# Kernel tuning notes

Measured on AMD Instinct MI355X. Metric: run time of the kernel, lower is better.

Reference implementation:

```python
import jax, jax.numpy as jnp
import numpy as np

NUM_LAYERS = 16
IN_SIZE = 1024
OUT_SIZE = 1024
B, S = 64, 128

def setup_inputs() -> dict:
    key = jax.random.key(0)
    k1, k2, k3 = jax.random.split(key, 3)
    x = jax.random.normal(k1, (B, S, IN_SIZE), dtype=jnp.float32)
    layer_idx = jax.random.randint(k2, (S,), 0, NUM_LAYERS)
    weight = jax.random.normal(k3, (NUM_LAYERS, OUT_SIZE, IN_SIZE), dtype=jnp.float32)
    return {"x": x, "layer_idx": layer_idx, "weight": weight}

def reference(x, layer_idx, weight):
    # Branch: layer_idx is 1D with len == S (per-position weight selection).
    # Gather per-position weights [S, O, D] and do one batched contraction,
    # equivalent to the Python loop of per-step matmuls in the original.
    w = weight[layer_idx]                       # [S, O, D]
    out = jnp.einsum('bsd,sod->bso', x, w)      # [B, S, O]
    return out
```

## Files before the change

### kernel.cpp

```cpp
#include <hip/hip_runtime.h>
#include <hip/hip_bf16.h>

#define B_ 64
#define S_ 128
#define D_ 1024
#define O_ 1024
#define L_ 16

typedef __bf16 bf16x8 __attribute__((ext_vector_type(8)));
typedef float f32x4 __attribute__((ext_vector_type(4)));

#define WS_W   0ull
#define WS_X   33554432ull
#define WS_P   50331648ull
#define WS_NEED (50331664ull + 72ull * 16ull)

__device__ __forceinline__ unsigned f2bf2(float a, float b) {
    union { float f; unsigned u; } x{a}, y{b};
    unsigned lo = x.u + 0x7FFFu + ((x.u >> 16) & 1u);
    unsigned hi = y.u + 0x7FFFu + ((y.u >> 16) & 1u);
    return (lo >> 16) | (hi & 0xFFFF0000u);
}

__device__ __forceinline__ void gload16(const void* g, void* l) {
    __builtin_amdgcn_global_load_lds(
        (const __attribute__((address_space(1))) void*)g,
        (__attribute__((address_space(3))) void*)l, 16, 0, 0);
}

__global__ __launch_bounds__(256) void moshi_convert(
    const float* __restrict__ x, const float* __restrict__ w,
    const int* __restrict__ lidx, unsigned char* __restrict__ ws) {
    if (blockIdx.x == 0 && threadIdx.x < 16) {
        int t = threadIdx.x;
        int cnt[16];
        #pragma unroll 1
        for (int m = 0; m < 16; ++m) cnt[m] = 0;
        for (int s = 0; s < S_; ++s) ++cnt[lidx[s]];
        int off = 0;
        for (int m = 0; m < t; ++m) off += (cnt[m] + 1) >> 1;
        int4* pairs = (int4*)(ws + WS_P + 16);
        int k = 0, prev = -1;
        for (int s = 0; s < S_; ++s) {
            if (lidx[s] == t) {
                if (k & 1) pairs[off + (k >> 1)] = make_int4(prev, s, t, 0);
                prev = s; ++k;
            }
        }
        if (k & 1) pairs[off + (k >> 1)] = make_int4(prev, prev, t, 0);
        if (t == 0) {
            int tot = 0;
            for (int m = 0; m < 16; ++m) tot += (cnt[m] + 1) >> 1;
            *(int*)(ws + WS_P) = tot;
        }
    }
    const float4* src;
    uint2* dst;
    unsigned i0 = blockIdx.x * 512 + threadIdx.x;
    if (blockIdx.x < 8192) {
        src = reinterpret_cast<const float4*>(w);
        dst = reinterpret_cast<uint2*>(ws + WS_W);
    } else {
        src = reinterpret_cast<const float4*>(x);
        dst = reinterpret_cast<uint2*>(ws + WS_X);
        i0 -= 4194304u;
    }
    float4 v0 = src[i0];
    float4 v1 = src[i0 + 256];
    dst[i0]       = make_uint2(f2bf2(v0.x, v0.y), f2bf2(v0.z, v0.w));
    dst[i0 + 256] = make_uint2(f2bf2(v1.x, v1.y), f2bf2(v1.z, v1.w));
}

__global__ __launch_bounds__(512, 4) void moshi_gemm_n128(
    const unsigned char* __restrict__ ws, float* __restrict__ out) {
    __shared__ __align__(16) unsigned char lw[16384];
    __shared__ __align__(16) unsigned char lx[16384];

    const int bid = (blockIdx.x & 7) * 72 + (blockIdx.x >> 3);
    const int pi = bid >> 3;
    const int nt = bid & 7;
    const int np = *reinterpret_cast<const int*>(ws + WS_P);
    if (pi >= np) return;
    const int4 pr = *reinterpret_cast<const int4*>(ws + WS_P + 16 + 16ull * pi);
    const int s0 = pr.x, s1 = pr.y, l = pr.z;

    const int tid = threadIdx.x, lane = tid & 63, wid = tid >> 6;

    const int rowq = tid >> 3;
    const int c16  = (tid & 7) << 4;
    const int csw  = c16 ^ ((rowq & 7) << 4);
    const unsigned char* wsrc0 = ws + WS_W
        + ((size_t)(l * 1024 + nt * 128 + rowq) << 11) + csw;
    const unsigned char* wsrc1 = wsrc0 + ((size_t)64 << 11);
    const unsigned char* xsrc0 = ws + WS_X
        + ((size_t)(rowq * 128 + s0) << 11) + csw;
    const unsigned char* xsrc1 = ws + WS_X
        + ((size_t)(rowq * 128 + s1) << 11) + csw;

    const int wm = wid >> 2, wn = wid & 3;
    const int swz = (lane & 7) << 4;
    const int kb  = (lane >> 4) << 4;
    const int a_base = (wm * 64 + (lane & 15)) * 128 + kb;
    const int b_base = (wn * 32 + (lane & 15)) * 128 + kb;

    f32x4 acc[4][2];
    #pragma unroll
    for (int i = 0; i < 4; ++i)
        #pragma unroll
        for (int j = 0; j < 2; ++j) acc[i][j] = (f32x4)0.0f;

    #pragma unroll 1
    for (int kt = 0; kt < 16; ++kt) {
        __syncthreads();
        gload16(wsrc0 + kt * 128, lw + tid * 16);
        gload16(wsrc1 + kt * 128, lw + tid * 16 + 8192);
        gload16(xsrc0 + kt * 128, lx + tid * 16);
        gload16(xsrc1 + kt * 128, lx + tid * 16 + 8192);
        __syncthreads();
        #pragma unroll
        for (int kk = 0; kk < 2; ++kk) {
            bf16x8 af[4], bfr[2];
            #pragma unroll
            for (int mi = 0; mi < 4; ++mi)
                af[mi] = *reinterpret_cast<const bf16x8*>(
                    lx + (((a_base + kk * 64) ^ swz) + mi * 2048));
            #pragma unroll
            for (int ni = 0; ni < 2; ++ni)
                bfr[ni] = *reinterpret_cast<const bf16x8*>(
                    lw + (((b_base + kk * 64) ^ swz) + ni * 2048));
            #pragma unroll
            for (int mi = 0; mi < 4; ++mi)
                #pragma unroll
                for (int ni = 0; ni < 2; ++ni)
                    acc[mi][ni] = __builtin_amdgcn_mfma_f32_16x16x32_bf16(
                        af[mi], bfr[ni], acc[mi][ni], 0, 0, 0);
        }
    }

    const int s_sel = wm ? s1 : s0;
    const int col0 = nt * 128 + wn * 32 + (lane & 15);
    const int r0 = (lane >> 4) << 2;
    #pragma unroll
    for (int mi = 0; mi < 4; ++mi)
        #pragma unroll
        for (int ni = 0; ni < 2; ++ni)
            #pragma unroll
            for (int r = 0; r < 4; ++r) {
                int b = mi * 16 + r0 + r;
                out[((size_t)b * S_ + s_sel) * O_ + col0 + ni * 16] = acc[mi][ni][r];
            }
}

__global__ __launch_bounds__(256) void moshi_flin_fallback(
    const float* __restrict__ x, const int* __restrict__ lidx,
    const float* __restrict__ w, float* __restrict__ out) {
    __shared__ __align__(16) unsigned char lxs[64 * 128];
    __shared__ __align__(16) unsigned char lws[128 * 128];
    const int bid = blockIdx.x;
    const int s = bid >> 3, n0 = (bid & 7) << 7;
    const int tid = threadIdx.x, lane = tid & 63, wid = tid >> 6;
    const int idx = lidx[s];
    const float* wb = w + (size_t)idx * O_ * D_ + (size_t)n0 * D_;
    const float* xb = x + (size_t)s * D_;
    const int swz = (lane & 7) << 4;
    const int kb = (lane >> 4) << 4;
    const int a_base = (lane & 15) * 128 + kb;
    const int b_base = (wid * 32 + (lane & 15)) * 128 + kb;
    f32x4 acc[4][2];
    #pragma unroll
    for (int i = 0; i < 4; ++i)
        #pragma unroll
        for (int j = 0; j < 2; ++j) acc[i][j] = (f32x4)0.0f;
    for (int kt = 0; kt < D_; kt += 64) {
        __syncthreads();
        #pragma unroll
        for (int p = 0; p < 4; ++p) {
            int f = tid + p * 256, row = f >> 4, cc = (f & 15) << 2;
            const float4 v = *reinterpret_cast<const float4*>(
                xb + (size_t)row * (S_ * D_) + kt + cc);
            uint2 pk = { f2bf2(v.x, v.y), f2bf2(v.z, v.w) };
            *reinterpret_cast<uint2*>(&lxs[(row * 128 + cc * 2) ^ ((row & 7) << 4)]) = pk;
        }
        #pragma unroll
        for (int p = 0; p < 8; ++p) {
            int f = tid + p * 256, row = f >> 4, cc = (f & 15) << 2;
            const float4 v = *reinterpret_cast<const float4*>(
                wb + (size_t)row * D_ + kt + cc);
            uint2 pk = { f2bf2(v.x, v.y), f2bf2(v.z, v.w) };
            *reinterpret_cast<uint2*>(&lws[(row * 128 + cc * 2) ^ ((row & 7) << 4)]) = pk;
        }
        __syncthreads();
        #pragma unroll
        for (int kk = 0; kk < 2; ++kk) {
            bf16x8 af[4], bfr[2];
            #pragma unroll
            for (int mi = 0; mi < 4; ++mi)
                af[mi] = *reinterpret_cast<const bf16x8*>(
                    &lxs[(((a_base + kk * 64) ^ swz) + mi * 2048)]);
            #pragma unroll
            for (int ni = 0; ni < 2; ++ni)
                bfr[ni] = *reinterpret_cast<const bf16x8*>(
                    &lws[(((b_base + kk * 64) ^ swz) + ni * 2048)]);
            #pragma unroll
            for (int mi = 0; mi < 4; ++mi)
                #pragma unroll
                for (int ni = 0; ni < 2; ++ni)
                    acc[mi][ni] = __builtin_amdgcn_mfma_f32_16x16x32_bf16(
                        af[mi], bfr[ni], acc[mi][ni], 0, 0, 0);
        }
    }
    float* ob = out + (size_t)s * O_ + n0 + wid * 32 + (lane & 15);
    const int r0 = (lane >> 4) << 2;
    #pragma unroll
    for (int mi = 0; mi < 4; ++mi)
        #pragma unroll
        for (int ni = 0; ni < 2; ++ni)
            #pragma unroll
            for (int r = 0; r < 4; ++r) {
                int b = mi * 16 + r0 + r;
                ob[(size_t)b * (S_ * O_) + ni * 16] = acc[mi][ni][r];
            }
}

extern "C" void kernel_launch(void* const* d_in, const int* in_sizes, int n_in,
                              void* d_out, int out_size, void* d_ws, size_t ws_size,
                              hipStream_t stream) {
    const float* x  = (const float*)d_in[0];
    const int* lidx = (const int*)d_in[1];
    const float* w  = (const float*)d_in[2];
    float* out      = (float*)d_out;

    if (ws_size < WS_NEED) {
        moshi_flin_fallback<<<dim3(128 * 8), dim3(256), 0, stream>>>(x, lidx, w, out);
        return;
    }
    unsigned char* ws = (unsigned char*)d_ws;
    moshi_convert<<<dim3(12288), dim3(256), 0, stream>>>(x, w, lidx, ws);
    moshi_gemm_n128<<<dim3(72 * 8), dim3(512), 0, stream>>>(ws, out);
}
```

Before: 56.29 us.

## Use atomic work queue per N-tile and transpose x to s-major bf16 layout

The GEMM now launches 512 persistent blocks that take pair work items from per-N-tile atomic counters, replacing the fixed 576-block grid where blocks beyond the pair count exit early. The convert kernel now writes x in [s][b][d] order, so the 64 batch rows for one position are contiguous, and it zeroes the queue counters. The aim is better load balance and more local x reads, at the cost of atomics and extra block-wide barriers per item.

```diff
diff --git a/kernel.cpp b/kernel.cpp
--- a/kernel.cpp
+++ b/kernel.cpp
@@ -10,10 +10,12 @@
 typedef __bf16 bf16x8 __attribute__((ext_vector_type(8)));
 typedef float f32x4 __attribute__((ext_vector_type(4)));
 
-#define WS_W   0ull
-#define WS_X   33554432ull
-#define WS_P   50331648ull
-#define WS_NEED (50331664ull + 72ull * 16ull)
+#define WS_W     0ull
+#define WS_X     33554432ull
+#define WS_P     50331648ull
+#define WS_PAIRS (WS_P + 16ull)
+#define WS_Q     (WS_PAIRS + 72ull * 16ull)
+#define WS_NEED  (WS_Q + 32ull)
 
 __device__ __forceinline__ unsigned f2bf2(float a, float b) {
     union { float f; unsigned u; } x{a}, y{b};
@@ -31,124 +33,142 @@
 __global__ __launch_bounds__(256) void moshi_convert(
     const float* __restrict__ x, const float* __restrict__ w,
     const int* __restrict__ lidx, unsigned char* __restrict__ ws) {
-    if (blockIdx.x == 0 && threadIdx.x < 16) {
-        int t = threadIdx.x;
-        int cnt[16];
-        #pragma unroll 1
-        for (int m = 0; m < 16; ++m) cnt[m] = 0;
-        for (int s = 0; s < S_; ++s) ++cnt[lidx[s]];
-        int off = 0;
-        for (int m = 0; m < t; ++m) off += (cnt[m] + 1) >> 1;
-        int4* pairs = (int4*)(ws + WS_P + 16);
-        int k = 0, prev = -1;
-        for (int s = 0; s < S_; ++s) {
-            if (lidx[s] == t) {
-                if (k & 1) pairs[off + (k >> 1)] = make_int4(prev, s, t, 0);
-                prev = s; ++k;
-            }
-        }
-        if (k & 1) pairs[off + (k >> 1)] = make_int4(prev, prev, t, 0);
-        if (t == 0) {
-            int tot = 0;
-            for (int m = 0; m < 16; ++m) tot += (cnt[m] + 1) >> 1;
-            *(int*)(ws + WS_P) = tot;
-        }
-    }
-    const float4* src;
-    uint2* dst;
+    if (blockIdx.x == 0 && threadIdx.x < 24) {
+        if (threadIdx.x >= 16) {
+            ((int*)(ws + WS_Q))[threadIdx.x - 16] = 0;
+        } else {
+            int t = threadIdx.x;
+            int cnt[16];
+            #pragma unroll 1
+            for (int m = 0; m < 16; ++m) cnt[m] = 0;
+            for (int s = 0; s < S_; ++s) ++cnt[lidx[s]];
+            int off = 0;
+            for (int m = 0; m < t; ++m) off += (cnt[m] + 1) >> 1;
+            int4* pairs = (int4*)(ws + WS_PAIRS);
+            int k = 0, prev = -1;
+            for (int s = 0; s < S_; ++s) {
+                if (lidx[s] == t) {
+                    if (k & 1) pairs[off + (k >> 1)] = make_int4(prev, s, t, 0);
+                    prev = s; ++k;
+                }
+            }
+            if (k & 1) pairs[off + (k >> 1)] = make_int4(prev, prev, t, 0);
+            if (t == 0) {
+                int tot = 0;
+                for (int m = 0; m < 16; ++m) tot += (cnt[m] + 1) >> 1;
+                *(int*)(ws + WS_P) = tot;
+            }
+        }
+    }
     unsigned i0 = blockIdx.x * 512 + threadIdx.x;
     if (blockIdx.x < 8192) {
-        src = reinterpret_cast<const float4*>(w);
-        dst = reinterpret_cast<uint2*>(ws + WS_W);
+        const float4* src = reinterpret_cast<const float4*>(w);
+        uint2* dst = reinterpret_cast<uint2*>(ws + WS_W);
+        float4 v0 = src[i0];
+        float4 v1 = src[i0 + 256];
+        dst[i0]       = make_uint2(f2bf2(v0.x, v0.y), f2bf2(v0.z, v0.w));
+        dst[i0 + 256] = make_uint2(f2bf2(v1.x, v1.y), f2bf2(v1.z, v1.w));
     } else {
-        src = reinterpret_cast<const float4*>(x);
-        dst = reinterpret_cast<uint2*>(ws + WS_X);
-        i0 -= 4194304u;
-    }
-    float4 v0 = src[i0];
-    float4 v1 = src[i0 + 256];
-    dst[i0]       = make_uint2(f2bf2(v0.x, v0.y), f2bf2(v0.z, v0.w));
-    dst[i0 + 256] = make_uint2(f2bf2(v1.x, v1.y), f2bf2(v1.z, v1.w));
-}
-
-__global__ __launch_bounds__(512, 4) void moshi_gemm_n128(
+        const float4* src = reinterpret_cast<const float4*>(x);
+        uint2* dst = reinterpret_cast<uint2*>(ws + WS_X);
+        unsigned j = i0 - 4194304u;
+        float4 v0 = src[j];
+        float4 v1 = src[j + 256];
+        unsigned b0 = j >> 15, s0 = (j >> 8) & 127u, d40 = j & 255u;
+        dst[(s0 * 64u + b0) * 256u + d40] =
+            make_uint2(f2bf2(v0.x, v0.y), f2bf2(v0.z, v0.w));
+        unsigned j1 = j + 256u;
+        unsigned b1 = j1 >> 15, s1 = (j1 >> 8) & 127u, d41 = j1 & 255u;
+        dst[(s1 * 64u + b1) * 256u + d41] =
+            make_uint2(f2bf2(v1.x, v1.y), f2bf2(v1.z, v1.w));
+    }
+}
+
+__global__ __launch_bounds__(512, 4) void moshi_gemm_pq(
     const unsigned char* __restrict__ ws, float* __restrict__ out) {
     __shared__ __align__(16) unsigned char lw[16384];
     __shared__ __align__(16) unsigned char lx[16384];
-
-    const int bid = (blockIdx.x & 7) * 72 + (blockIdx.x >> 3);
-    const int pi = bid >> 3;
-    const int nt = bid & 7;
+    __shared__ int item_s;
+
+    const int nt = blockIdx.x & 7;
+    int* ctr = (int*)(ws + WS_Q) + nt;
     const int np = *reinterpret_cast<const int*>(ws + WS_P);
-    if (pi >= np) return;
-    const int4 pr = *reinterpret_cast<const int4*>(ws + WS_P + 16 + 16ull * pi);
-    const int s0 = pr.x, s1 = pr.y, l = pr.z;
 
     const int tid = threadIdx.x, lane = tid & 63, wid = tid >> 6;
-
     const int rowq = tid >> 3;
     const int c16  = (tid & 7) << 4;
     const int csw  = c16 ^ ((rowq & 7) << 4);
-    const unsigned char* wsrc0 = ws + WS_W
-        + ((size_t)(l * 1024 + nt * 128 + rowq) << 11) + csw;
-    const unsigned char* wsrc1 = wsrc0 + ((size_t)64 << 11);
-    const unsigned char* xsrc0 = ws + WS_X
-        + ((size_t)(rowq * 128 + s0) << 11) + csw;
-    const unsigned char* xsrc1 = ws + WS_X
-        + ((size_t)(rowq * 128 + s1) << 11) + csw;
-
     const int wm = wid >> 2, wn = wid & 3;
     const int swz = (lane & 7) << 4;
     const int kb  = (lane >> 4) << 4;
     const int a_base = (wm * 64 + (lane & 15)) * 128 + kb;
     const int b_base = (wn * 32 + (lane & 15)) * 128 + kb;
 
-    f32x4 acc[4][2];
-    #pragma unroll
-    for (int i = 0; i < 4; ++i)
-        #pragma unroll
-        for (int j = 0; j < 2; ++j) acc[i][j] = (f32x4)0.0f;
-
-    #pragma unroll 1
-    for (int kt = 0; kt < 16; ++kt) {
-        __syncthreads();
-        gload16(wsrc0 + kt * 128, lw + tid * 16);
-        gload16(wsrc1 + kt * 128, lw + tid * 16 + 8192);
-        gload16(xsrc0 + kt * 128, lx + tid * 16);
-        gload16(xsrc1 + kt * 128, lx + tid * 16 + 8192);
-        __syncthreads();
-        #pragma unroll
-        for (int kk = 0; kk < 2; ++kk) {
-            bf16x8 af[4], bfr[2];
-            #pragma unroll
-            for (int mi = 0; mi < 4; ++mi)
-                af[mi] = *reinterpret_cast<const bf16x8*>(
-                    lx + (((a_base + kk * 64) ^ swz) + mi * 2048));
+    const unsigned char* wbase = ws + WS_W + ((size_t)(nt * 128 + rowq) << 11) + csw;
+
+    for (;;) {
+        if (tid == 0) item_s = atomicAdd(ctr, 1);
+        __syncthreads();
+        const int pi = item_s;
+        __syncthreads();
+        if (pi >= 72) break;
+        if (pi >= np) continue;
+
+        const int4 pr = *reinterpret_cast<const int4*>(ws + WS_PAIRS + 16ull * pi);
+        const int s0 = pr.x, s1 = pr.y, l = pr.z;
+
+        const unsigned char* wsrc0 = wbase + ((size_t)(l * 1024) << 11);
+        const unsigned char* wsrc1 = wsrc0 + ((size_t)64 << 11);
+        const unsigned char* xsrc0 = ws + WS_X + ((size_t)(s0 * 64 + rowq) << 11) + csw;
+        const unsigned char* xsrc1 = ws + WS_X + ((size_t)(s1 * 64 + rowq) << 11) + csw;
+
+        f32x4 acc[4][2];
+        #pragma unroll
+        for (int i = 0; i < 4; ++i)
+            #pragma unroll
+            for (int j = 0; j < 2; ++j) acc[i][j] = (f32x4)0.0f;
+
+        #pragma unroll 1
+        for (int kt = 0; kt < 16; ++kt) {
+            __syncthreads();
+            gload16(wsrc0 + kt * 128, lw + tid * 16);
+            gload16(wsrc1 + kt * 128, lw + tid * 16 + 8192);
+            gload16(xsrc0 + kt * 128, lx + tid * 16);
+            gload16(xsrc1 + kt * 128, lx + tid * 16 + 8192);
+            __syncthreads();
+            #pragma unroll
+            for (int kk = 0; kk < 2; ++kk) {
+                bf16x8 af[4], bfr[2];
+                #pragma unroll
+                for (int mi = 0; mi < 4; ++mi)
+                    af[mi] = *reinterpret_cast<const bf16x8*>(
+                        lx + (((a_base + kk * 64) ^ swz) + mi * 2048));
+                #pragma unroll
+                for (int ni = 0; ni < 2; ++ni)
+                    bfr[ni] = *reinterpret_cast<const bf16x8*>(
+                        lw + (((b_base + kk * 64) ^ swz) + ni * 2048));
+                #pragma unroll
+                for (int mi = 0; mi < 4; ++mi)
+                    #pragma unroll
+                    for (int ni = 0; ni < 2; ++ni)
+                        acc[mi][ni] = __builtin_amdgcn_mfma_f32_16x16x32_bf16(
+                            af[mi], bfr[ni], acc[mi][ni], 0, 0, 0);
+            }
+        }
+
+        const int s_sel = wm ? s1 : s0;
+        const int col0 = nt * 128 + wn * 32 + (lane & 15);
+        const int r0 = (lane >> 4) << 2;
+        #pragma unroll
+        for (int mi = 0; mi < 4; ++mi)
             #pragma unroll
             for (int ni = 0; ni < 2; ++ni)
-                bfr[ni] = *reinterpret_cast<const bf16x8*>(
-                    lw + (((b_base + kk * 64) ^ swz) + ni * 2048));
-            #pragma unroll
-            for (int mi = 0; mi < 4; ++mi)
-                #pragma unroll
-                for (int ni = 0; ni < 2; ++ni)
-                    acc[mi][ni] = __builtin_amdgcn_mfma_f32_16x16x32_bf16(
-                        af[mi], bfr[ni], acc[mi][ni], 0, 0, 0);
-        }
-    }
-
-    const int s_sel = wm ? s1 : s0;
-    const int col0 = nt * 128 + wn * 32 + (lane & 15);
-    const int r0 = (lane >> 4) << 2;
-    #pragma unroll
-    for (int mi = 0; mi < 4; ++mi)
-        #pragma unroll
-        for (int ni = 0; ni < 2; ++ni)
-            #pragma unroll
-            for (int r = 0; r < 4; ++r) {
-                int b = mi * 16 + r0 + r;
-                out[((size_t)b * S_ + s_sel) * O_ + col0 + ni * 16] = acc[mi][ni][r];
-            }
+                #pragma unroll
+                for (int r = 0; r < 4; ++r) {
+                    int b = mi * 16 + r0 + r;
+                    out[((size_t)b * S_ + s_sel) * O_ + col0 + ni * 16] = acc[mi][ni][r];
+                }
+    }
 }
 
 __global__ __launch_bounds__(256) void moshi_flin_fallback(
@@ -236,5 +256,5 @@
     }
     unsigned char* ws = (unsigned char*)d_ws;
     moshi_convert<<<dim3(12288), dim3(256), 0, stream>>>(x, w, lidx, ws);
-    moshi_gemm_n128<<<dim3(72 * 8), dim3(512), 0, stream>>>(ws, out);
-}
+    moshi_gemm_pq<<<dim3(512), dim3(512), 0, stream>>>(ws, out);
+}
```

Result: slower. 75.11 us (+33.4%).

## Pre-pack x into MFMA fragment layout and load A operands directly from global

Applied to the files above, without the earlier changes.

The convert kernel now writes bf16 x in a per-position layout that matches the MFMA A-fragment order, so each lane can read its fragments with one 16-byte global load. The GEMM kernel drops the x shared-memory tile and its staging loads, keeping only the weight tile in LDS. The aim is to cut LDS traffic and shared memory use, which may raise occupancy. In exchange, A operands come straight from global or cache with latency exposed inside the k loop, and the convert kernel's stores become scattered.

```diff
diff --git a/kernel.cpp b/kernel.cpp
--- a/kernel.cpp
+++ b/kernel.cpp
@@ -9,11 +9,13 @@
 
 typedef __bf16 bf16x8 __attribute__((ext_vector_type(8)));
 typedef float f32x4 __attribute__((ext_vector_type(4)));
-
-#define WS_W   0ull
-#define WS_X   33554432ull
-#define WS_P   50331648ull
-#define WS_NEED (50331664ull + 72ull * 16ull)
+typedef unsigned u32x4 __attribute__((ext_vector_type(4)));
+
+#define WS_W     0ull
+#define WS_X     33554432ull
+#define WS_P     50331648ull
+#define WS_PAIRS (WS_P + 16ull)
+#define WS_NEED  (WS_PAIRS + 72ull * 16ull)
 
 __device__ __forceinline__ unsigned f2bf2(float a, float b) {
     union { float f; unsigned u; } x{a}, y{b};
@@ -39,7 +41,7 @@
         for (int s = 0; s < S_; ++s) ++cnt[lidx[s]];
         int off = 0;
         for (int m = 0; m < t; ++m) off += (cnt[m] + 1) >> 1;
-        int4* pairs = (int4*)(ws + WS_P + 16);
+        int4* pairs = (int4*)(ws + WS_PAIRS);
         int k = 0, prev = -1;
         for (int s = 0; s < S_; ++s) {
             if (lidx[s] == t) {
@@ -54,54 +56,56 @@
             *(int*)(ws + WS_P) = tot;
         }
     }
-    const float4* src;
-    uint2* dst;
-    unsigned i0 = blockIdx.x * 512 + threadIdx.x;
     if (blockIdx.x < 8192) {
-        src = reinterpret_cast<const float4*>(w);
-        dst = reinterpret_cast<uint2*>(ws + WS_W);
+        unsigned i0 = blockIdx.x * 512u + threadIdx.x;
+        const float4* src = reinterpret_cast<const float4*>(w);
+        uint2* dst = reinterpret_cast<uint2*>(ws + WS_W);
+        float4 v0 = src[i0];
+        float4 v1 = src[i0 + 256];
+        dst[i0]       = make_uint2(f2bf2(v0.x, v0.y), f2bf2(v0.z, v0.w));
+        dst[i0 + 256] = make_uint2(f2bf2(v1.x, v1.y), f2bf2(v1.z, v1.w));
     } else {
-        src = reinterpret_cast<const float4*>(x);
-        dst = reinterpret_cast<uint2*>(ws + WS_X);
-        i0 -= 4194304u;
-    }
-    float4 v0 = src[i0];
-    float4 v1 = src[i0 + 256];
-    dst[i0]       = make_uint2(f2bf2(v0.x, v0.y), f2bf2(v0.z, v0.w));
-    dst[i0 + 256] = make_uint2(f2bf2(v1.x, v1.y), f2bf2(v1.z, v1.w));
-}
-
-__global__ __launch_bounds__(512, 4) void moshi_gemm_n128(
+        unsigned p = (blockIdx.x - 8192u) * 256u + threadIdx.x;
+        const float4* src = reinterpret_cast<const float4*>(x);
+        float4 v0 = src[2u * p];
+        float4 v1 = src[2u * p + 1u];
+        unsigned b = p >> 14, s = (p >> 7) & 127u, d8 = p & 127u;
+        unsigned kt = d8 >> 3, kk = (d8 >> 2) & 1u, lh = d8 & 3u;
+        unsigned mi = b >> 4, ml = b & 15u;
+        unsigned dstb = s * 131072u + (((kt * 2u + kk) * 4u + mi) << 10)
+                      + ((ml + lh * 16u) << 4);
+        u32x4 pk = { f2bf2(v0.x, v0.y), f2bf2(v0.z, v0.w),
+                     f2bf2(v1.x, v1.y), f2bf2(v1.z, v1.w) };
+        *reinterpret_cast<u32x4*>(ws + WS_X + dstb) = pk;
+    }
+}
+
+__global__ __launch_bounds__(512, 4) void moshi_gemm_xd(
     const unsigned char* __restrict__ ws, float* __restrict__ out) {
     __shared__ __align__(16) unsigned char lw[16384];
-    __shared__ __align__(16) unsigned char lx[16384];
 
     const int bid = (blockIdx.x & 7) * 72 + (blockIdx.x >> 3);
     const int pi = bid >> 3;
     const int nt = bid & 7;
     const int np = *reinterpret_cast<const int*>(ws + WS_P);
     if (pi >= np) return;
-    const int4 pr = *reinterpret_cast<const int4*>(ws + WS_P + 16 + 16ull * pi);
+    const int4 pr = *reinterpret_cast<const int4*>(ws + WS_PAIRS + 16ull * pi);
     const int s0 = pr.x, s1 = pr.y, l = pr.z;
 
     const int tid = threadIdx.x, lane = tid & 63, wid = tid >> 6;
-
     const int rowq = tid >> 3;
     const int c16  = (tid & 7) << 4;
     const int csw  = c16 ^ ((rowq & 7) << 4);
     const unsigned char* wsrc0 = ws + WS_W
         + ((size_t)(l * 1024 + nt * 128 + rowq) << 11) + csw;
     const unsigned char* wsrc1 = wsrc0 + ((size_t)64 << 11);
-    const unsigned char* xsrc0 = ws + WS_X
-        + ((size_t)(rowq * 128 + s0) << 11) + csw;
-    const unsigned char* xsrc1 = ws + WS_X
-        + ((size_t)(rowq * 128 + s1) << 11) + csw;
 
     const int wm = wid >> 2, wn = wid & 3;
     const int swz = (lane & 7) << 4;
     const int kb  = (lane >> 4) << 4;
-    const int a_base = (wm * 64 + (lane & 15)) * 128 + kb;
     const int b_base = (wn * 32 + (lane & 15)) * 128 + kb;
+    const int s_sel = wm ? s1 : s0;
+    const unsigned char* xA = ws + WS_X + (size_t)s_sel * 131072 + lane * 16;
 
     f32x4 acc[4][2];
     #pragma unroll
@@ -114,16 +118,17 @@
         __syncthreads();
         gload16(wsrc0 + kt * 128, lw + tid * 16);
         gload16(wsrc1 + kt * 128, lw + tid * 16 + 8192);
-        gload16(xsrc0 + kt * 128, lx + tid * 16);
-        gload16(xsrc1 + kt * 128, lx + tid * 16 + 8192);
+        bf16x8 af[2][4];
+        #pragma unroll
+        for (int kk = 0; kk < 2; ++kk)
+            #pragma unroll
+            for (int mi = 0; mi < 4; ++mi)
+                af[kk][mi] = *reinterpret_cast<const bf16x8*>(
+                    xA + (((kt * 2 + kk) * 4 + mi) << 10));
         __syncthreads();
         #pragma unroll
         for (int kk = 0; kk < 2; ++kk) {
-            bf16x8 af[4], bfr[2];
-            #pragma unroll
-            for (int mi = 0; mi < 4; ++mi)
-                af[mi] = *reinterpret_cast<const bf16x8*>(
-                    lx + (((a_base + kk * 64) ^ swz) + mi * 2048));
+            bf16x8 bfr[2];
             #pragma unroll
             for (int ni = 0; ni < 2; ++ni)
                 bfr[ni] = *reinterpret_cast<const bf16x8*>(
@@ -133,11 +138,10 @@
                 #pragma unroll
                 for (int ni = 0; ni < 2; ++ni)
                     acc[mi][ni] = __builtin_amdgcn_mfma_f32_16x16x32_bf16(
-                        af[mi], bfr[ni], acc[mi][ni], 0, 0, 0);
-        }
-    }
-
-    const int s_sel = wm ? s1 : s0;
+                        af[kk][mi], bfr[ni], acc[mi][ni], 0, 0, 0);
+        }
+    }
+
     const int col0 = nt * 128 + wn * 32 + (lane & 15);
     const int r0 = (lane >> 4) << 2;
     #pragma unroll
@@ -236,5 +240,5 @@
     }
     unsigned char* ws = (unsigned char*)d_ws;
     moshi_convert<<<dim3(12288), dim3(256), 0, stream>>>(x, w, lidx, ws);
-    moshi_gemm_n128<<<dim3(72 * 8), dim3(512), 0, stream>>>(ws, out);
-}
+    moshi_gemm_xd<<<dim3(72 * 8), dim3(512), 0, stream>>>(ws, out);
+}
```

New measurement: 75.31 us. 1.34x slower.
